# Kernel optimization log

Measured on AMD Instinct MI355X. Metric: run time of the kernel, lower is better.

Reference implementation:

```python
import jax, jax.numpy as jnp
import numpy as np

EPS_LN = 1e-6
EPS_NORM = 1e-12
MAX_SCALE_MUL = float(np.log(100.0))
H = 16  # num_heads


def _ln(x):
    # affine-free LayerNorm over last dim (torch uses biased variance)
    mu = jnp.mean(x, axis=-1, keepdims=True)
    var = jnp.mean((x - mu) ** 2, axis=-1, keepdims=True)
    return (x - mu) / jnp.sqrt(var + EPS_LN)


def _l2norm(x):
    n = jnp.sqrt(jnp.sum(x * x, axis=-1, keepdims=True))
    return x / jnp.maximum(n, EPS_NORM)


def setup_inputs() -> dict:
    key = jax.random.key(0)
    ks = jax.random.split(key, 12)
    B, L, C = 4, 1024, 1024
    Ccond, Dff = 1024, 4096
    s = lambda fan: 1.0 / np.sqrt(fan)
    return {
        "x": jax.random.normal(ks[0], (B, L, C), jnp.float32),
        "cond": jax.random.normal(ks[1], (B, Ccond), jnp.float32),
        "mat_qkv_w": jax.random.normal(ks[2], (3 * C, C), jnp.float32) * s(C),
        "q_bias": jnp.zeros((C,), jnp.float32),
        "v_bias": jnp.zeros((C,), jnp.float32),
        "scale_mul": jnp.full((1, H, 1, 1), np.log(4.0), jnp.float32),
        "proj_w": jax.random.normal(ks[3], (C, C), jnp.float32) * s(C),
        "proj_b": jnp.zeros((C,), jnp.float32),
        "ada_w": jax.random.normal(ks[4], (6 * C, Ccond), jnp.float32) * s(Ccond),
        "ada_b": jnp.zeros((6 * C,), jnp.float32),
        "fc1_w": jax.random.normal(ks[5], (Dff, C), jnp.float32) * s(C),
        "fc1_b": jnp.zeros((Dff,), jnp.float32),
        "fc2_w": jax.random.normal(ks[6], (C, Dff), jnp.float32) * s(Dff),
        "fc2_b": jnp.zeros((C,), jnp.float32),
    }


def reference(x, cond, mat_qkv_w, q_bias, v_bias, scale_mul, proj_w, proj_b,
              ada_w, ada_b, fc1_w, fc1_b, fc2_w, fc2_b):
    B, L, C = x.shape
    hd = C // H

    # AdaLN modulation params: SiLU -> Linear -> [B,1,6,C]
    ada = jax.nn.silu(cond) @ ada_w.T + ada_b
    ada = ada.reshape(B, 1, 6, C)
    gamma1, gamma2, scale1, scale2, shift1, shift2 = [ada[:, :, i] for i in range(6)]

    # --- attention branch ---
    x1 = _ln(x) * (scale1 + 1.0) + shift1
    qkv_bias = jnp.concatenate([q_bias, jnp.zeros_like(q_bias), v_bias])
    qkv = (x1 @ mat_qkv_w.T + qkv_bias).reshape(B, L, 3, H, hd)
    q, k, v = [jnp.transpose(qkv[:, :, i], (0, 2, 1, 3)) for i in range(3)]  # [B,H,L,hd]

    sm = jnp.exp(jnp.minimum(scale_mul, MAX_SCALE_MUL))  # [1,H,1,1]
    q = _l2norm(q) * sm
    k = _l2norm(k)

    scores = jnp.einsum('bhqd,bhkd->bhqk', q, k)  # scale = 1.0 under l2 norm
    probs = jax.nn.softmax(scores, axis=-1)
    o = jnp.einsum('bhqk,bhkd->bhqd', probs, v)
    o = jnp.transpose(o, (0, 2, 1, 3)).reshape(B, L, C)
    attn_out = o @ proj_w.T + proj_b
    x = x + attn_out * gamma1

    # --- FFN branch ---
    x2 = _ln(x) * (scale2 + 1.0) + shift2
    h = jax.nn.gelu(x2 @ fc1_w.T + fc1_b, approximate=False)
    ffn_out = h @ fc2_w.T + fc2_b
    x = x + ffn_out * gamma2
    return x
```

## Files before the change

### kernel.cpp

```cpp
#include <hip/hip_runtime.h>

typedef __bf16 bf16x8_t __attribute__((ext_vector_type(8)));
typedef bf16x8_t bf16x8 __attribute__((may_alias));
typedef float f32x4 __attribute__((ext_vector_type(4)));
typedef unsigned short u16x4 __attribute__((ext_vector_type(4)));
typedef unsigned short u16x8 __attribute__((ext_vector_type(8)));

#define DEV __device__ __forceinline__

DEV float b2f(unsigned short u) {
  union { unsigned int i; float f; } x; x.i = ((unsigned int)u) << 16; return x.f;
}
DEV unsigned short f2b(float f) {
  union { float f; unsigned int i; } x; x.f = f;
  return (unsigned short)((x.i + 0x7fffu + ((x.i >> 16) & 1u)) >> 16);
}

#define AS1(p) ((__attribute__((address_space(1))) void*)(p))
#define AS3(p) ((__attribute__((address_space(3))) void*)(p))

__global__ void k_silu(const float* __restrict__ c, float* __restrict__ o) {
  int i = blockIdx.x * 256 + threadIdx.x;
  float v = c[i];
  o[i] = v / (1.f + __expf(-v));
}

__global__ __launch_bounds__(256) void k_ada(const float* __restrict__ sc,
                                             const float* __restrict__ w,
                                             const float* __restrict__ bias,
                                             float* __restrict__ out) {
  int j = blockIdx.x * 4 + (threadIdx.x >> 6);
  int lane = threadIdx.x & 63;
  const float* wr = w + (size_t)j * 1024;
  float s0 = 0.f, s1 = 0.f, s2 = 0.f, s3 = 0.f;
#pragma unroll
  for (int u = 0; u < 4; ++u) {
    int k = u * 256 + lane * 4;
    float4 a = *(const float4*)(wr + k);
    float4 c0 = *(const float4*)(sc + k);
    float4 c1 = *(const float4*)(sc + 1024 + k);
    float4 c2 = *(const float4*)(sc + 2048 + k);
    float4 c3 = *(const float4*)(sc + 3072 + k);
    s0 += a.x * c0.x + a.y * c0.y + a.z * c0.z + a.w * c0.w;
    s1 += a.x * c1.x + a.y * c1.y + a.z * c1.z + a.w * c1.w;
    s2 += a.x * c2.x + a.y * c2.y + a.z * c2.z + a.w * c2.w;
    s3 += a.x * c3.x + a.y * c3.y + a.z * c3.z + a.w * c3.w;
  }
#pragma unroll
  for (int o = 1; o < 64; o <<= 1) {
    s0 += __shfl_xor(s0, o); s1 += __shfl_xor(s1, o);
    s2 += __shfl_xor(s2, o); s3 += __shfl_xor(s3, o);
  }
  if (lane == 0) {
    float bb = bias[j];
    out[j] = s0 + bb;
    out[6144 + j] = s1 + bb;
    out[12288 + j] = s2 + bb;
    out[18432 + j] = s3 + bb;
  }
}

__global__ void k_cast(const float* __restrict__ s, unsigned short* __restrict__ d, int n) {
  int i = (blockIdx.x * 256 + threadIdx.x) * 4;
  if (i >= n) return;
  float4 v = *(const float4*)(s + i);
  u16x4 o;
  o[0] = f2b(v.x); o[1] = f2b(v.y); o[2] = f2b(v.z); o[3] = f2b(v.w);
  *(u16x4*)(d + i) = o;
}

__global__ __launch_bounds__(256) void k_ln_mod(const float* __restrict__ src,
                                                const float* __restrict__ ada,
                                                unsigned short* __restrict__ dst,
                                                int sidx, int hidx) {
  int row = blockIdx.x;
  int b = row >> 10;
  int t = threadIdx.x, lane = t & 63, wv = t >> 6;
  float4 v = *(const float4*)(src + (size_t)row * 1024 + t * 4);
  float s = v.x + v.y + v.z + v.w;
  float s2 = v.x * v.x + v.y * v.y + v.z * v.z + v.w * v.w;
#pragma unroll
  for (int o = 1; o < 64; o <<= 1) { s += __shfl_xor(s, o); s2 += __shfl_xor(s2, o); }
  __shared__ float red[8];
  if (lane == 0) { red[wv] = s; red[4 + wv] = s2; }
  __syncthreads();
  float ts = red[0] + red[1] + red[2] + red[3];
  float ts2 = red[4] + red[5] + red[6] + red[7];
  float mu = ts * (1.f / 1024.f);
  float var = ts2 * (1.f / 1024.f) - mu * mu;
  float rstd = rsqrtf(var + 1e-6f);
  const float* ar = ada + (size_t)b * 6144;
  float4 sc = *(const float4*)(ar + sidx * 1024 + t * 4);
  float4 sh = *(const float4*)(ar + hidx * 1024 + t * 4);
  u16x4 o;
  o[0] = f2b((v.x - mu) * rstd * (sc.x + 1.f) + sh.x);
  o[1] = f2b((v.y - mu) * rstd * (sc.y + 1.f) + sh.y);
  o[2] = f2b((v.z - mu) * rstd * (sc.z + 1.f) + sh.z);
  o[3] = f2b((v.w - mu) * rstd * (sc.w + 1.f) + sh.w);
  *(u16x4*)(dst + (size_t)row * 1024 + t * 4) = o;
}

template <int EPI>
__global__ __launch_bounds__(512, 2) void k_gemm256(const unsigned short* __restrict__ A,
                                                    const unsigned short* __restrict__ W,
                                                    int M, int N, int K,
                                                    const float* __restrict__ bias,
                                                    const float* __restrict__ qb,
                                                    const float* __restrict__ vb,
                                                    void* __restrict__ outp) {
  __shared__ unsigned short LDS[65536];
  const int tid = threadIdx.x;
  const int wv = tid >> 6, lane = tid & 63;
  const int fr = lane & 15, fg = lane >> 4;
  const int wm = wv >> 2, wn = wv & 3;

  const int nx = N >> 8;
  const int cpx = gridDim.x >> 3;
  const int wid = ((int)blockIdx.x & 7) * cpx + ((int)blockIdx.x >> 3);
  const int m0 = (wid / nx) * 256, n0 = (wid % nx) * 256;

  const int srow = tid >> 2;
  const int sgc = (tid & 3) ^ ((srow >> 1) & 3);
  const unsigned short* srcA = A + (size_t)(m0 + srow) * K + sgc * 8;
  const unsigned short* srcB = W + (size_t)(n0 + srow) * K + sgc * 8;

#define STG256(t_, h_)                                                                        \
  __builtin_amdgcn_global_load_lds(                                                           \
      AS1(((h_) < 2 ? srcA : srcB) + (size_t)((h_)&1) * 128 * K + (size_t)(t_) * 32),         \
      AS3(LDS + ((t_)&3) * 16384 + ((h_) >> 1) * 8192 + ((h_)&1) * 4096 + wv * 512), 16, 0, 0)

  f32x4 zz = {0.f, 0.f, 0.f, 0.f};
  f32x4 acc[8][4];
#pragma unroll
  for (int i = 0; i < 8; ++i)
#pragma unroll
    for (int j = 0; j < 4; ++j) acc[i][j] = zz;

  const int xc = (fg ^ ((fr >> 1) & 3)) * 8;
  const int aoff = (wm * 128 + fr) * 32 + xc;
  const int boff = 8192 + (wn * 64 + fr) * 32 + xc;

  const int nt = K >> 5;

#pragma unroll
  for (int t2 = 0; t2 < 3; ++t2) {
    STG256(t2, 0); STG256(t2, 1); STG256(t2, 2); STG256(t2, 3);
  }
  asm volatile("s_waitcnt vmcnt(8)" ::: "memory");
  __builtin_amdgcn_s_barrier();

#define LDSV(off) (*(const bf16x8*)(LDS + (off)))
#define MM2(r0, r1, aX0, aX1)                                                                 \
  {                                                                                           \
    _Pragma("unroll") for (int ni = 0; ni < 4; ++ni) {                                        \
      acc[r0][ni] = __builtin_amdgcn_mfma_f32_16x16x32_bf16(aX0, bfr[ni], acc[r0][ni], 0, 0, 0); \
      acc[r1][ni] = __builtin_amdgcn_mfma_f32_16x16x32_bf16(aX1, bfr[ni], acc[r1][ni], 0, 0, 0); \
    }                                                                                         \
  }

  for (int t = 0; t < nt; ++t) {
    const int bufo = (t & 3) * 16384;
    const bool more = (t + 3) < nt;
    bf16x8 bfr[4], aA0, aA1, aB0, aB1;
#pragma unroll
    for (int ni = 0; ni < 4; ++ni) bfr[ni] = LDSV(bufo + boff + ni * 512);
    aA0 = LDSV(bufo + aoff);
    aA1 = LDSV(bufo + aoff + 512);
    aB0 = LDSV(bufo + aoff + 2 * 512);
    aB1 = LDSV(bufo + aoff + 3 * 512);
    if (more) STG256(t + 3, 0);
    __builtin_amdgcn_s_setprio(1);
    MM2(0, 1, aA0, aA1);
    __builtin_amdgcn_s_setprio(0);
    __builtin_amdgcn_s_barrier();
    aA0 = LDSV(bufo + aoff + 4 * 512);
    aA1 = LDSV(bufo + aoff + 5 * 512);
    if (more) STG256(t + 3, 1);
    __builtin_amdgcn_s_setprio(1);
    MM2(2, 3, aB0, aB1);
    __builtin_amdgcn_s_setprio(0);
    __builtin_amdgcn_s_barrier();
    aB0 = LDSV(bufo + aoff + 6 * 512);
    aB1 = LDSV(bufo + aoff + 7 * 512);
    if (more) STG256(t + 3, 2);
    __builtin_amdgcn_s_setprio(1);
    MM2(4, 5, aA0, aA1);
    __builtin_amdgcn_s_setprio(0);
    __builtin_amdgcn_s_barrier();
    if (more) STG256(t + 3, 3);
    __builtin_amdgcn_s_setprio(1);
    MM2(6, 7, aB0, aB1);
    __builtin_amdgcn_s_setprio(0);
    if (t < nt - 1) {
      if (t <= nt - 4) {
        asm volatile("s_waitcnt vmcnt(8)" ::: "memory");
      } else if (t == nt - 3) {
        asm volatile("s_waitcnt vmcnt(4)" ::: "memory");
      } else {
        asm volatile("s_waitcnt vmcnt(0)" ::: "memory");
      }
      __builtin_amdgcn_s_barrier();
    }
  }

#pragma unroll
  for (int mi = 0; mi < 8; ++mi) {
#pragma unroll
    for (int ni = 0; ni < 4; ++ni) {
#pragma unroll
      for (int r = 0; r < 4; ++r) {
        int m = m0 + wm * 128 + mi * 16 + fg * 4 + r;
        int n = n0 + wn * 64 + ni * 16 + fr;
        float v = acc[mi][ni][r];
        if constexpr (EPI == 0) {
          float bb = (n < 1024) ? qb[n] : ((n < 2048) ? 0.f : vb[n - 2048]);
          ((unsigned short*)outp)[(size_t)m * N + n] = f2b(v + bb);
        } else {
          float z = v + bias[n];
          ((unsigned short*)outp)[(size_t)m * N + n] =
              f2b(0.5f * z * (1.f + erff(z * 0.70710678118654752f)));
        }
      }
    }
  }
#undef STG256
#undef LDSV
#undef MM2
}

template <int EPI>
__global__ __launch_bounds__(512) void k_gemm8(const unsigned short* __restrict__ A,
                                               const unsigned short* __restrict__ W,
                                               int M, int N, int K, int Khalf,
                                               const float* __restrict__ bias,
                                               const float* __restrict__ resid,
                                               const float* __restrict__ ada,
                                               float* __restrict__ outp) {
  __shared__ unsigned short SM[49152];
  const int t = threadIdx.x, lane = t & 63, wv = t >> 6;
  const int grp = wv >> 2, w4 = wv & 3;
  const int wr = w4 >> 1, wc = w4 & 1;
  const int cpx = gridDim.x >> 3;
  const int orig = blockIdx.x;
  const int wid = (orig & 7) * cpx + (orig >> 3);
  const int nx = N >> 7;
  const int m0 = (wid / nx) * 128, n0 = (wid % nx) * 128;

  f32x4 zz = {0.f, 0.f, 0.f, 0.f};
  f32x4 acc[4][4];
#pragma unroll
  for (int i = 0; i < 4; ++i)
#pragma unroll
    for (int j = 0; j < 4; ++j) acc[i][j] = zz;

  const int srow = lane >> 2, scol = (lane & 3) * 8;
  const int kbase = grp * Khalf;
  const unsigned short* aSrc0 = A + (size_t)(m0 + w4 * 16 + srow) * K + kbase + scol;
  const unsigned short* aSrc1 = aSrc0 + (size_t)64 * K;
  const unsigned short* bSrc0 = W + (size_t)(n0 + w4 * 16 + srow) * K + kbase + scol;
  const unsigned short* bSrc1 = bSrc0 + (size_t)64 * K;
  unsigned short* grpA = SM + grp * 24576;

  const int fr = lane & 15, fk = (lane >> 4) * 8;

#define STG8(buf_, k0_)                                                                            \
  {                                                                                                \
    __builtin_amdgcn_global_load_lds(AS1(aSrc0 + (k0_)), AS3(grpA + (buf_)*8192 + w4 * 512), 16, 0, 0); \
    __builtin_amdgcn_global_load_lds(AS1(aSrc1 + (k0_)), AS3(grpA + (buf_)*8192 + 2048 + w4 * 512), 16, 0, 0); \
    __builtin_amdgcn_global_load_lds(AS1(bSrc0 + (k0_)), AS3(grpA + (buf_)*8192 + 4096 + w4 * 512), 16, 0, 0); \
    __builtin_amdgcn_global_load_lds(AS1(bSrc1 + (k0_)), AS3(grpA + (buf_)*8192 + 6144 + w4 * 512), 16, 0, 0); \
  }

  const int nsteps = Khalf >> 5;
  STG8(0, 0);
  STG8(1, 32);
  asm volatile("s_waitcnt vmcnt(4)" ::: "memory");
  __builtin_amdgcn_s_barrier();

  for (int i = 0; i < nsteps; ++i) {
    const int buf = i % 3;
    if (i + 2 < nsteps) STG8((i + 2) % 3, (i + 2) * 32);
    const unsigned short* aRd = grpA + buf * 8192 + (wr * 64 + fr) * 32 + fk;
    const unsigned short* bRd = grpA + buf * 8192 + 4096 + (wc * 64 + fr) * 32 + fk;
    bf16x8 af[4], bfv[4];
#pragma unroll
    for (int q = 0; q < 4; ++q) af[q] = *(const bf16x8*)(aRd + q * 512);
#pragma unroll
    for (int q = 0; q < 4; ++q) bfv[q] = *(const bf16x8*)(bRd + q * 512);
#pragma unroll
    for (int mi = 0; mi < 4; ++mi)
#pragma unroll
      for (int ni = 0; ni < 4; ++ni)
        acc[mi][ni] = __builtin_amdgcn_mfma_f32_16x16x32_bf16(af[mi], bfv[ni], acc[mi][ni], 0, 0, 0);
    if (i < nsteps - 1) {
      if (i + 2 < nsteps) {
        asm volatile("s_waitcnt vmcnt(4)" ::: "memory");
      } else {
        asm volatile("s_waitcnt vmcnt(0)" ::: "memory");
      }
      __builtin_amdgcn_s_barrier();
    }
  }
  __syncthreads();

  float* xch = (float*)SM;
#pragma unroll
  for (int c = 0; c < 16; ++c) {
    if (grp == 1)
      *(f32x4*)&xch[c * 1024 + (w4 * 64 + lane) * 4] = acc[c >> 2][c & 3];
  }
  __syncthreads();
  if (grp == 1) return;
#pragma unroll
  for (int c = 0; c < 16; ++c) {
    f32x4 p = *(const f32x4*)&xch[c * 1024 + (w4 * 64 + lane) * 4];
    acc[c >> 2][c & 3] += p;
  }

  const int fg = lane >> 4;
#pragma unroll
  for (int mi = 0; mi < 4; ++mi) {
#pragma unroll
    for (int ni = 0; ni < 4; ++ni) {
#pragma unroll
      for (int r = 0; r < 4; ++r) {
        int m = m0 + wr * 64 + mi * 16 + fg * 4 + r;
        int n = n0 + wc * 64 + ni * 16 + fr;
        float v = acc[mi][ni][r];
        const int aoff = (EPI == 1) ? 0 : 1024;
        float g = ada[(size_t)(m >> 10) * 6144 + aoff + n];
        outp[(size_t)m * N + n] = resid[(size_t)m * N + n] + (v + bias[n]) * g;
      }
    }
  }
#undef STG8
}

__global__ __launch_bounds__(256) void k_qknorm(const unsigned short* __restrict__ qkv,
                                                const float* __restrict__ smul,
                                                unsigned short* __restrict__ Qn,
                                                unsigned short* __restrict__ Kn) {
  int row = blockIdx.x;
  int b = row >> 10, l = row & 1023;
  int t = threadIdx.x;
  int h = t >> 4, sl = t & 15;
  const unsigned short* base = qkv + (size_t)row * 3072 + h * 64 + sl * 4;
  size_t off = ((size_t)(b * 16 + h) * 1024 + l) * 64 + sl * 4;
  {
    u16x4 qv = *(const u16x4*)base;
    float q0 = b2f(qv[0]), q1 = b2f(qv[1]), q2 = b2f(qv[2]), q3 = b2f(qv[3]);
    float ss = q0 * q0 + q1 * q1 + q2 * q2 + q3 * q3;
#pragma unroll
    for (int o = 1; o < 16; o <<= 1) ss += __shfl_xor(ss, o);
    float sm = __expf(fminf(smul[h], 4.6051701859880914f));
    float qs = sm / fmaxf(sqrtf(ss), 1e-12f);
    u16x4 o; o[0] = f2b(q0 * qs); o[1] = f2b(q1 * qs); o[2] = f2b(q2 * qs); o[3] = f2b(q3 * qs);
    *(u16x4*)(Qn + off) = o;
  }
  {
    u16x4 kv = *(const u16x4*)(base + 1024);
    float k0 = b2f(kv[0]), k1 = b2f(kv[1]), k2 = b2f(kv[2]), k3 = b2f(kv[3]);
    float ss = k0 * k0 + k1 * k1 + k2 * k2 + k3 * k3;
#pragma unroll
    for (int o = 1; o < 16; o <<= 1) ss += __shfl_xor(ss, o);
    float ks = 1.f / fmaxf(sqrtf(ss), 1e-12f);
    u16x4 o; o[0] = f2b(k0 * ks); o[1] = f2b(k1 * ks); o[2] = f2b(k2 * ks); o[3] = f2b(k3 * ks);
    *(u16x4*)(Kn + off) = o;
  }
}

__global__ __launch_bounds__(256) void k_vtrans(const unsigned short* __restrict__ qkv,
                                                unsigned short* __restrict__ Vt) {
  int bh = blockIdx.y, b = bh >> 4, h = bh & 15;
  int l0 = blockIdx.x * 64;
  __shared__ unsigned short tile[64][72];
  int t = threadIdx.x;
  int lr = t >> 2, dp = (t & 3) * 16;
  const unsigned short* src = qkv + (size_t)(b * 1024 + l0 + lr) * 3072 + 2048 + h * 64 + dp;
  *(u16x8*)&tile[lr][dp] = *(const u16x8*)src;
  *(u16x8*)&tile[lr][dp + 8] = *(const u16x8*)(src + 8);
  __syncthreads();
  int d = t >> 2, lp = (t & 3) * 16;
  unsigned short ov[16];
#pragma unroll
  for (int j = 0; j < 16; ++j) {
    int p = lp + j;
    int l = ((p >> 5) * 2 + ((p >> 2) & 1)) * 16 + ((p >> 3) & 3) * 4 + (p & 3);
    ov[j] = tile[l][d];
  }
  unsigned short* dst = Vt + ((size_t)bh * 64 + d) * 1024 + l0 + lp;
  *(u16x8*)dst = *(u16x8*)&ov[0];
  *(u16x8*)(dst + 8) = *(u16x8*)&ov[8];
}

__global__ __launch_bounds__(256) void k_attn(const unsigned short* __restrict__ Qn,
                                              const unsigned short* __restrict__ Kn,
                                              const unsigned short* __restrict__ Vt,
                                              const float* __restrict__ smul,
                                              unsigned short* __restrict__ O) {
  const int qt = blockIdx.x, bh = blockIdx.y;
  const int b = bh >> 4, h = bh & 15;
  const int t = threadIdx.x, lane = t & 63, wv = t >> 6;
  const int fr = lane & 15, fg = lane >> 4;
  __shared__ unsigned short Kb[2][4096];
  __shared__ unsigned short Vb[2][4096];

  const int q0 = qt * 128 + wv * 32;
  const unsigned short* qp = Qn + ((size_t)bh * 1024 + q0 + fr) * 64 + fg * 8;
  bf16x8 qf00 = *(const bf16x8*)qp;
  bf16x8 qf01 = *(const bf16x8*)(qp + 32);
  bf16x8 qf10 = *(const bf16x8*)(qp + 1024);
  bf16x8 qf11 = *(const bf16x8*)(qp + 1024 + 32);

  const float M = __expf(fminf(smul[h], 4.6051701859880914f));

  const int srow = lane >> 3, sc = lane & 7;
  const int xr = (sc ^ srow) * 8;
  const unsigned short* kp0 = Kn + (size_t)bh * 65536 + (size_t)(wv * 16 + srow) * 64 + xr;
  const unsigned short* kp1 = kp0 + 8 * 64;
  const unsigned short* vp0 = Vt + (size_t)bh * 65536 + (size_t)(wv * 16 + srow) * 1024 + xr;
  const unsigned short* vp1 = vp0 + 8 * 1024;

  f32x4 zz = {0.f, 0.f, 0.f, 0.f};
  f32x4 oa0[4], oa1[4];
#pragma unroll
  for (int i = 0; i < 4; ++i) { oa0[i] = zz; oa1[i] = zz; }
  float ls0 = 0.f, ls1 = 0.f;

  {
    unsigned short* kd = &Kb[0][wv * 1024];
    unsigned short* vd = &Vb[0][wv * 1024];
    __builtin_amdgcn_global_load_lds(AS1(kp0), AS3(kd), 16, 0, 0);
    __builtin_amdgcn_global_load_lds(AS1(kp1), AS3(kd + 512), 16, 0, 0);
    __builtin_amdgcn_global_load_lds(AS1(vp0), AS3(vd), 16, 0, 0);
    __builtin_amdgcn_global_load_lds(AS1(vp1), AS3(vd + 512), 16, 0, 0);
  }
  __syncthreads();

  int cur = 0;
  for (int kv = 0; kv < 1024; kv += 64) {
    const int nxt = cur ^ 1;
    if (kv + 64 < 1024) {
      const int ko = (kv + 64) * 64;
      const int vo = kv + 64;
      unsigned short* kd = &Kb[nxt][wv * 1024];
      unsigned short* vd = &Vb[nxt][wv * 1024];
      __builtin_amdgcn_global_load_lds(AS1(kp0 + ko), AS3(kd), 16, 0, 0);
      __builtin_amdgcn_global_load_lds(AS1(kp1 + ko), AS3(kd + 512), 16, 0, 0);
      __builtin_amdgcn_global_load_lds(AS1(vp0 + vo), AS3(vd), 16, 0, 0);
      __builtin_amdgcn_global_load_lds(AS1(vp1 + vo), AS3(vd + 512), 16, 0, 0);
    }

    f32x4 s0[4], s1[4];
#pragma unroll
    for (int ct = 0; ct < 4; ++ct) {
      const int row = ct * 16 + fr, r7 = row & 7;
      const unsigned short* kr = &Kb[cur][row * 64];
      bf16x8 kf0 = *(const bf16x8*)(kr + ((fg ^ r7) << 3));
      bf16x8 kf1 = *(const bf16x8*)(kr + (((4 + fg) ^ r7) << 3));
      f32x4 z0 = __builtin_amdgcn_mfma_f32_16x16x32_bf16(kf0, qf00, zz, 0, 0, 0);
      s0[ct] = __builtin_amdgcn_mfma_f32_16x16x32_bf16(kf1, qf01, z0, 0, 0, 0);
      f32x4 z1 = __builtin_amdgcn_mfma_f32_16x16x32_bf16(kf0, qf10, zz, 0, 0, 0);
      s1[ct] = __builtin_amdgcn_mfma_f32_16x16x32_bf16(kf1, qf11, z1, 0, 0, 0);
    }

    bf16x8 pa0[2], pa1[2];
#pragma unroll
    for (int kg = 0; kg < 2; ++kg) {
      bf16x8 a0, a1;
#pragma unroll
      for (int c2 = 0; c2 < 2; ++c2) {
#pragma unroll
        for (int r = 0; r < 4; ++r) {
          float e0 = __expf(s0[kg * 2 + c2][r] - M);
          float e1 = __expf(s1[kg * 2 + c2][r] - M);
          ls0 += e0; ls1 += e1;
          a0[c2 * 4 + r] = (__bf16)e0;
          a1[c2 * 4 + r] = (__bf16)e1;
        }
      }
      pa0[kg] = a0; pa1[kg] = a1;
    }

#pragma unroll
    for (int kg = 0; kg < 2; ++kg) {
#pragma unroll
      for (int dt = 0; dt < 4; ++dt) {
        const int row = dt * 16 + fr, r7 = row & 7;
        bf16x8 vf = *(const bf16x8*)(&Vb[cur][row * 64] + ((((kg << 2) + fg) ^ r7) << 3));
        oa0[dt] = __builtin_amdgcn_mfma_f32_16x16x32_bf16(pa0[kg], vf, oa0[dt], 0, 0, 0);
        oa1[dt] = __builtin_amdgcn_mfma_f32_16x16x32_bf16(pa1[kg], vf, oa1[dt], 0, 0, 0);
      }
    }
    __syncthreads();
    cur = nxt;
  }

  ls0 += __shfl_xor(ls0, 16); ls0 += __shfl_xor(ls0, 32);
  ls1 += __shfl_xor(ls1, 16); ls1 += __shfl_xor(ls1, 32);

#pragma unroll
  for (int r = 0; r < 4; ++r) {
    float i0 = 1.f / __shfl(ls0, fg * 4 + r);
    float i1 = 1.f / __shfl(ls1, fg * 4 + r);
    unsigned short* ob = O + ((size_t)(b * 1024 + q0 + fg * 4 + r)) * 1024 + h * 64 + fr;
#pragma unroll
    for (int dt = 0; dt < 4; ++dt) {
      ob[dt * 16] = f2b(oa0[dt][r] * i0);
      ob[(size_t)16 * 1024 + dt * 16] = f2b(oa1[dt][r] * i1);
    }
  }
}

extern "C" void kernel_launch(void* const* d_in, const int* in_sizes, int n_in,
                              void* d_out, int out_size, void* d_ws, size_t ws_size,
                              hipStream_t stream) {
  const float* x        = (const float*)d_in[0];
  const float* cond     = (const float*)d_in[1];
  const float* qkv_w    = (const float*)d_in[2];
  const float* q_bias   = (const float*)d_in[3];
  const float* v_bias   = (const float*)d_in[4];
  const float* scale_mul= (const float*)d_in[5];
  const float* proj_w   = (const float*)d_in[6];
  const float* proj_b   = (const float*)d_in[7];
  const float* ada_w    = (const float*)d_in[8];
  const float* ada_b    = (const float*)d_in[9];
  const float* fc1_w    = (const float*)d_in[10];
  const float* fc1_b    = (const float*)d_in[11];
  const float* fc2_w    = (const float*)d_in[12];
  const float* fc2_b    = (const float*)d_in[13];
  float* out = (float*)d_out;
  char* ws = (char*)d_ws;

  unsigned short* WQ   = (unsigned short*)(ws + 0);
  unsigned short* WP   = (unsigned short*)(ws + 6291456);
  unsigned short* WF1  = (unsigned short*)(ws + 8388608);
  unsigned short* WF2  = (unsigned short*)(ws + 16777216);
  float*          SIL  = (float*)(ws + 25165824);
  float*          ADA  = (float*)(ws + 25182208);
  unsigned short* X1   = (unsigned short*)(ws + 25280512);
  unsigned short* QKVB = (unsigned short*)(ws + 33669120);
  unsigned short* QN   = (unsigned short*)(ws + 58834944);
  unsigned short* KN   = (unsigned short*)(ws + 67223552);
  unsigned short* VT   = (unsigned short*)(ws + 75612160);
  unsigned short* OB   = (unsigned short*)(ws + 84000768);
  float*          XMID = (float*)(ws + 33669120);
  unsigned short* HB   = (unsigned short*)(ws + 50446336);

  (void)in_sizes; (void)n_in; (void)out_size; (void)ws_size;

  k_silu<<<16, 256, 0, stream>>>(cond, SIL);
  k_ada<<<1536, 256, 0, stream>>>(SIL, ada_w, ada_b, ADA);
  k_cast<<<3072, 256, 0, stream>>>(qkv_w, WQ, 3145728);
  k_cast<<<1024, 256, 0, stream>>>(proj_w, WP, 1048576);
  k_cast<<<4096, 256, 0, stream>>>(fc1_w, WF1, 4194304);
  k_cast<<<4096, 256, 0, stream>>>(fc2_w, WF2, 4194304);

  k_ln_mod<<<4096, 256, 0, stream>>>(x, ADA, X1, 2, 4);
  k_gemm256<0><<<192, 512, 0, stream>>>(X1, WQ, 4096, 3072, 1024,
                                        nullptr, q_bias, v_bias, QKVB);
  k_qknorm<<<4096, 256, 0, stream>>>(QKVB, scale_mul, QN, KN);
  k_vtrans<<<dim3(16, 64), 256, 0, stream>>>(QKVB, VT);
  k_attn<<<dim3(8, 64), 256, 0, stream>>>(QN, KN, VT, scale_mul, OB);
  k_gemm8<1><<<256, 512, 0, stream>>>(OB, WP, 4096, 1024, 1024, 512,
                                      proj_b, x, ADA, XMID);
  k_ln_mod<<<4096, 256, 0, stream>>>(XMID, ADA, X1, 3, 5);
  k_gemm256<2><<<256, 512, 0, stream>>>(X1, WF1, 4096, 4096, 1024,
                                        fc1_b, nullptr, nullptr, HB);
  k_gemm8<3><<<256, 512, 0, stream>>>(HB, WF2, 4096, 1024, 4096, 2048,
                                      fc2_b, XMID, ADA, out);
}
```

Before: 243.3 us.

## Restructure 256-tile GEMM loop, tanh GELU, split-K fc2 with reduction kernel

Rewrites the 256x256 GEMM main loop to stage A and B half-tiles separately, at a 64-wide K step with finer-grained barriers. It also adds a split-K mode that writes bf16 partials. The fc2 GEMM now runs as a 4-way split-K through this kernel, followed by a separate reduction kernel that applies bias, gate and residual. The exact erf GELU is replaced with the tanh approximation, and partial sums are rounded to bf16, which changes numerics.

```diff
diff --git a/kernel.cpp b/kernel.cpp
--- a/kernel.cpp
+++ b/kernel.cpp
@@ -100,34 +100,46 @@
   *(u16x4*)(dst + (size_t)row * 1024 + t * 4) = o;
 }
 
-template <int EPI>
+template <int EPI, int SPLIT>
 __global__ __launch_bounds__(512, 2) void k_gemm256(const unsigned short* __restrict__ A,
                                                     const unsigned short* __restrict__ W,
-                                                    int M, int N, int K,
+                                                    int N, int lda, int ldb, int nt,
                                                     const float* __restrict__ bias,
                                                     const float* __restrict__ qb,
                                                     const float* __restrict__ vb,
-                                                    void* __restrict__ outp) {
+                                                    unsigned short* __restrict__ o0,
+                                                    unsigned short* __restrict__ o1,
+                                                    unsigned short* __restrict__ o2,
+                                                    unsigned short* __restrict__ o3) {
   __shared__ unsigned short LDS[65536];
   const int tid = threadIdx.x;
   const int wv = tid >> 6, lane = tid & 63;
   const int fr = lane & 15, fg = lane >> 4;
   const int wm = wv >> 2, wn = wv & 3;
 
+  const int cpx = gridDim.x >> 3;
+  int wid = ((int)blockIdx.x & 7) * cpx + ((int)blockIdx.x >> 3);
+  int s = 0;
+  if (SPLIT > 1) { s = wid & (SPLIT - 1); wid >>= 2; }
   const int nx = N >> 8;
-  const int cpx = gridDim.x >> 3;
-  const int wid = ((int)blockIdx.x & 7) * cpx + ((int)blockIdx.x >> 3);
   const int m0 = (wid / nx) * 256, n0 = (wid % nx) * 256;
-
-  const int srow = tid >> 2;
-  const int sgc = (tid & 3) ^ ((srow >> 1) & 3);
-  const unsigned short* srcA = A + (size_t)(m0 + srow) * K + sgc * 8;
-  const unsigned short* srcB = W + (size_t)(n0 + srow) * K + sgc * 8;
-
-#define STG256(t_, h_)                                                                        \
-  __builtin_amdgcn_global_load_lds(                                                           \
-      AS1(((h_) < 2 ? srcA : srcB) + (size_t)((h_)&1) * 128 * K + (size_t)(t_) * 32),         \
-      AS3(LDS + ((t_)&3) * 16384 + ((h_) >> 1) * 8192 + ((h_)&1) * 4096 + wv * 512), 16, 0, 0)
+  const int kbase = s * (nt << 6);
+  unsigned short* outp = (SPLIT > 1) ? (s == 0 ? o0 : s == 1 ? o1 : s == 2 ? o2 : o3) : o0;
+
+  const int sRow = lane >> 2;
+  const int sCh = (lane & 3) ^ ((lane >> 3) & 3);
+  const unsigned short* aG = A + (size_t)(m0 + wv * 16 + sRow) * lda + kbase + sCh * 8;
+  const unsigned short* bG = W + (size_t)(n0 + wv * 16 + sRow) * ldb + kbase + sCh * 8;
+
+#define STQ(qi_, iop_, rh_)                                                                   \
+  __builtin_amdgcn_global_load_lds(                                                          \
+      AS1(((iop_) ? bG : aG) + (size_t)(rh_)*128 * ((iop_) ? ldb : lda) +                    \
+          (((qi_) >> 1) * 64 + ((qi_)&1) * 32)),                                             \
+      AS3(LDS + ((qi_)&3) * 16384 + (iop_)*8192 + (rh_)*4096 + wv * 512), 16, 0, 0)
+
+  const int rswz = (fr >> 1) & 3;
+  const int aRd = (wm * 128 + fr) * 32 + ((fg ^ rswz) << 3);
+  const int bRd = 8192 + (wn * 64 + fr) * 32 + ((fg ^ rswz) << 3);
 
   f32x4 zz = {0.f, 0.f, 0.f, 0.f};
   f32x4 acc[8][4];
@@ -136,68 +148,60 @@
 #pragma unroll
     for (int j = 0; j < 4; ++j) acc[i][j] = zz;
 
-  const int xc = (fg ^ ((fr >> 1) & 3)) * 8;
-  const int aoff = (wm * 128 + fr) * 32 + xc;
-  const int boff = 8192 + (wn * 64 + fr) * 32 + xc;
-
-  const int nt = K >> 5;
-
-#pragma unroll
-  for (int t2 = 0; t2 < 3; ++t2) {
-    STG256(t2, 0); STG256(t2, 1); STG256(t2, 2); STG256(t2, 3);
+#pragma unroll
+  for (int qq = 0; qq < 3; ++qq) {
+    STQ(qq, 0, 0); STQ(qq, 0, 1); STQ(qq, 1, 0); STQ(qq, 1, 1);
   }
   asm volatile("s_waitcnt vmcnt(8)" ::: "memory");
   __builtin_amdgcn_s_barrier();
 
 #define LDSV(off) (*(const bf16x8*)(LDS + (off)))
-#define MM2(r0, r1, aX0, aX1)                                                                 \
-  {                                                                                           \
-    _Pragma("unroll") for (int ni = 0; ni < 4; ++ni) {                                        \
-      acc[r0][ni] = __builtin_amdgcn_mfma_f32_16x16x32_bf16(aX0, bfr[ni], acc[r0][ni], 0, 0, 0); \
-      acc[r1][ni] = __builtin_amdgcn_mfma_f32_16x16x32_bf16(aX1, bfr[ni], acc[r1][ni], 0, 0, 0); \
-    }                                                                                         \
-  }
 
   for (int t = 0; t < nt; ++t) {
-    const int bufo = (t & 3) * 16384;
-    const bool more = (t + 3) < nt;
-    bf16x8 bfr[4], aA0, aA1, aB0, aB1;
-#pragma unroll
-    for (int ni = 0; ni < 4; ++ni) bfr[ni] = LDSV(bufo + boff + ni * 512);
-    aA0 = LDSV(bufo + aoff);
-    aA1 = LDSV(bufo + aoff + 512);
-    aB0 = LDSV(bufo + aoff + 2 * 512);
-    aB1 = LDSV(bufo + aoff + 3 * 512);
-    if (more) STG256(t + 3, 0);
-    __builtin_amdgcn_s_setprio(1);
-    MM2(0, 1, aA0, aA1);
-    __builtin_amdgcn_s_setprio(0);
-    __builtin_amdgcn_s_barrier();
-    aA0 = LDSV(bufo + aoff + 4 * 512);
-    aA1 = LDSV(bufo + aoff + 5 * 512);
-    if (more) STG256(t + 3, 1);
-    __builtin_amdgcn_s_setprio(1);
-    MM2(2, 3, aB0, aB1);
-    __builtin_amdgcn_s_setprio(0);
-    __builtin_amdgcn_s_barrier();
-    aB0 = LDSV(bufo + aoff + 6 * 512);
-    aB1 = LDSV(bufo + aoff + 7 * 512);
-    if (more) STG256(t + 3, 2);
-    __builtin_amdgcn_s_setprio(1);
-    MM2(4, 5, aA0, aA1);
-    __builtin_amdgcn_s_setprio(0);
-    __builtin_amdgcn_s_barrier();
-    if (more) STG256(t + 3, 3);
-    __builtin_amdgcn_s_setprio(1);
-    MM2(6, 7, aB0, aB1);
-    __builtin_amdgcn_s_setprio(0);
-    if (t < nt - 1) {
-      if (t <= nt - 4) {
-        asm volatile("s_waitcnt vmcnt(8)" ::: "memory");
-      } else if (t == nt - 3) {
-        asm volatile("s_waitcnt vmcnt(4)" ::: "memory");
-      } else {
-        asm volatile("s_waitcnt vmcnt(0)" ::: "memory");
+    bf16x8 bq0, bq1, bq2, bq3;
+#pragma unroll
+    for (int p = 0; p < 4; ++p) {
+      const int kk = p >> 1;
+      const int reg = ((2 * t + kk) & 3) * 16384;
+      if ((p & 1) == 0) {
+        bq0 = LDSV(reg + bRd);
+        bq1 = LDSV(reg + bRd + 512);
+        bq2 = LDSV(reg + bRd + 1024);
+        bq3 = LDSV(reg + bRd + 1536);
+      }
+      bf16x8 a0 = LDSV(reg + aRd + (p & 1) * 2048);
+      bf16x8 a1 = LDSV(reg + aRd + (p & 1) * 2048 + 512);
+      bf16x8 a2 = LDSV(reg + aRd + (p & 1) * 2048 + 1024);
+      bf16x8 a3 = LDSV(reg + aRd + (p & 1) * 2048 + 1536);
+      {
+        const int gph = 4 * t + p;
+        const int qi = (gph >> 1) + 3;
+        if (qi < 2 * nt) {
+          const int iop = gph & 1;
+          if (iop) { STQ(qi, 1, 0); STQ(qi, 1, 1); }
+          else     { STQ(qi, 0, 0); STQ(qi, 0, 1); }
+        }
+      }
+      __builtin_amdgcn_s_barrier();
+      asm volatile("s_waitcnt lgkmcnt(0)" ::: "memory");
+      __builtin_amdgcn_sched_barrier(0);
+      __builtin_amdgcn_s_setprio(1);
+      const int mg = (p & 1) * 4;
+#pragma unroll
+      for (int ni = 0; ni < 4; ++ni) {
+        bf16x8 bb = ni == 0 ? bq0 : ni == 1 ? bq1 : ni == 2 ? bq2 : bq3;
+        acc[mg + 0][ni] = __builtin_amdgcn_mfma_f32_16x16x32_bf16(a0, bb, acc[mg + 0][ni], 0, 0, 0);
+        acc[mg + 1][ni] = __builtin_amdgcn_mfma_f32_16x16x32_bf16(a1, bb, acc[mg + 1][ni], 0, 0, 0);
+        acc[mg + 2][ni] = __builtin_amdgcn_mfma_f32_16x16x32_bf16(a2, bb, acc[mg + 2][ni], 0, 0, 0);
+        acc[mg + 3][ni] = __builtin_amdgcn_mfma_f32_16x16x32_bf16(a3, bb, acc[mg + 3][ni], 0, 0, 0);
+      }
+      __builtin_amdgcn_s_setprio(0);
+      if (p == 1) {
+        if (t == nt - 1) { asm volatile("s_waitcnt vmcnt(0)" ::: "memory"); }
+        else             { asm volatile("s_waitcnt vmcnt(8)" ::: "memory"); }
+      } else if (p == 3 && t < nt - 1) {
+        if (t == nt - 2) { asm volatile("s_waitcnt vmcnt(4)" ::: "memory"); }
+        else             { asm volatile("s_waitcnt vmcnt(8)" ::: "memory"); }
       }
       __builtin_amdgcn_s_barrier();
     }
@@ -214,21 +218,49 @@
         float v = acc[mi][ni][r];
         if constexpr (EPI == 0) {
           float bb = (n < 1024) ? qb[n] : ((n < 2048) ? 0.f : vb[n - 2048]);
-          ((unsigned short*)outp)[(size_t)m * N + n] = f2b(v + bb);
+          outp[(size_t)m * N + n] = f2b(v + bb);
+        } else if constexpr (EPI == 2) {
+          float z = v + bias[n];
+          float u = z * (0.7978845608f + 0.0356774081f * z * z);
+          float e = __expf(2.f * u);
+          float th = 1.f - 2.f / (e + 1.f);
+          outp[(size_t)m * N + n] = f2b(0.5f * z * (1.f + th));
         } else {
-          float z = v + bias[n];
-          ((unsigned short*)outp)[(size_t)m * N + n] =
-              f2b(0.5f * z * (1.f + erff(z * 0.70710678118654752f)));
+          outp[(size_t)m * N + n] = f2b(v);
         }
       }
     }
   }
-#undef STG256
+#undef STQ
 #undef LDSV
-#undef MM2
-}
-
-template <int EPI>
+}
+
+__global__ __launch_bounds__(256) void k_fc2red(const unsigned short* __restrict__ P0,
+                                                const unsigned short* __restrict__ P1,
+                                                const unsigned short* __restrict__ P2,
+                                                const unsigned short* __restrict__ P3,
+                                                const float* __restrict__ xmid,
+                                                const float* __restrict__ bias,
+                                                const float* __restrict__ ada,
+                                                float* __restrict__ out) {
+  size_t idx = ((size_t)blockIdx.x * 256 + threadIdx.x) * 8;
+  int n = (int)(idx & 1023);
+  int b = (int)(idx >> 20);
+  u16x8 v0 = *(const u16x8*)(P0 + idx);
+  u16x8 v1 = *(const u16x8*)(P1 + idx);
+  u16x8 v2 = *(const u16x8*)(P2 + idx);
+  u16x8 v3 = *(const u16x8*)(P3 + idx);
+  const float* gp = ada + (size_t)b * 6144 + 1024 + n;
+  const float* bp = bias + n;
+  const float* xp = xmid + idx;
+  float* op = out + idx;
+#pragma unroll
+  for (int i = 0; i < 8; ++i) {
+    float sum = b2f(v0[i]) + b2f(v1[i]) + b2f(v2[i]) + b2f(v3[i]);
+    op[i] = xp[i] + (sum + bp[i]) * gp[i];
+  }
+}
+
 __global__ __launch_bounds__(512) void k_gemm8(const unsigned short* __restrict__ A,
                                                const unsigned short* __restrict__ W,
                                                int M, int N, int K, int Khalf,
@@ -327,8 +359,7 @@
         int m = m0 + wr * 64 + mi * 16 + fg * 4 + r;
         int n = n0 + wc * 64 + ni * 16 + fr;
         float v = acc[mi][ni][r];
-        const int aoff = (EPI == 1) ? 0 : 1024;
-        float g = ada[(size_t)(m >> 10) * 6144 + aoff + n];
+        float g = ada[(size_t)(m >> 10) * 6144 + n];
         outp[(size_t)m * N + n] = resid[(size_t)m * N + n] + (v + bias[n]) * g;
       }
     }
@@ -546,6 +577,10 @@
   unsigned short* OB   = (unsigned short*)(ws + 84000768);
   float*          XMID = (float*)(ws + 33669120);
   unsigned short* HB   = (unsigned short*)(ws + 50446336);
+  unsigned short* FP0  = (unsigned short*)(ws + 0);
+  unsigned short* FP1  = (unsigned short*)(ws + 8388608);
+  unsigned short* FP2  = (unsigned short*)(ws + 25280512);
+  unsigned short* FP3  = (unsigned short*)(ws + 84000768);
 
   (void)in_sizes; (void)n_in; (void)out_size; (void)ws_size;
 
@@ -557,16 +592,17 @@
   k_cast<<<4096, 256, 0, stream>>>(fc2_w, WF2, 4194304);
 
   k_ln_mod<<<4096, 256, 0, stream>>>(x, ADA, X1, 2, 4);
-  k_gemm256<0><<<192, 512, 0, stream>>>(X1, WQ, 4096, 3072, 1024,
-                                        nullptr, q_bias, v_bias, QKVB);
+  k_gemm256<0, 1><<<192, 512, 0, stream>>>(X1, WQ, 3072, 1024, 1024, 16,
+                                           nullptr, q_bias, v_bias, QKVB, nullptr, nullptr, nullptr);
   k_qknorm<<<4096, 256, 0, stream>>>(QKVB, scale_mul, QN, KN);
   k_vtrans<<<dim3(16, 64), 256, 0, stream>>>(QKVB, VT);
   k_attn<<<dim3(8, 64), 256, 0, stream>>>(QN, KN, VT, scale_mul, OB);
-  k_gemm8<1><<<256, 512, 0, stream>>>(OB, WP, 4096, 1024, 1024, 512,
-                                      proj_b, x, ADA, XMID);
+  k_gemm8<<<256, 512, 0, stream>>>(OB, WP, 4096, 1024, 1024, 512,
+                                   proj_b, x, ADA, XMID);
   k_ln_mod<<<4096, 256, 0, stream>>>(XMID, ADA, X1, 3, 5);
-  k_gemm256<2><<<256, 512, 0, stream>>>(X1, WF1, 4096, 4096, 1024,
-                                        fc1_b, nullptr, nullptr, HB);
-  k_gemm8<3><<<256, 512, 0, stream>>>(HB, WF2, 4096, 1024, 4096, 2048,
-                                      fc2_b, XMID, ADA, out);
-}
+  k_gemm256<2, 1><<<256, 512, 0, stream>>>(X1, WF1, 4096, 1024, 1024, 16,
+                                           fc1_b, nullptr, nullptr, HB, nullptr, nullptr, nullptr);
+  k_gemm256<4, 4><<<256, 512, 0, stream>>>(HB, WF2, 1024, 4096, 4096, 16,
+                                           nullptr, nullptr, nullptr, FP0, FP1, FP2, FP3);
+  k_fc2red<<<2048, 256, 0, stream>>>(FP0, FP1, FP2, FP3, XMID, fc2_b, ADA, out);
+}
```

After: 237.8 us. -2.3%, faster.
